# Optimization experiments

Hardware: AMD Instinct MI355X
Metric: run time of the kernel (lower is better)

## Reference

```python
import jax, jax.numpy as jnp
import numpy as np
from math import sqrt

HEADS = 16
DIM_HEAD = 64
BETA = 1.0 / sqrt(DIM_HEAD)


def setup_inputs() -> dict:
    key = jax.random.key(0)
    k1, k2, k3 = jax.random.split(key, 3)
    b, n, dim = 2, 2048, 1024
    inner = HEADS * DIM_HEAD  # 1024
    x = jax.random.normal(k1, (b, n, dim), dtype=jnp.float32)
    W_qk = jax.random.normal(k2, (dim, 2 * inner), dtype=jnp.float32) * 0.02
    W_out = jax.random.normal(k3, (inner, dim), dtype=jnp.float32) * 0.02
    return {"x": x, "W_qk": W_qk, "W_out": W_out}


def reference(x, W_qk, W_out):
    # x: [b, n, dim]; to_qk: Linear(dim, 2*inner, bias=False)
    b, n, _ = x.shape
    qk = x @ W_qk                                   # [b, n, 2*inner]
    q, k = jnp.split(qk, 2, axis=-1)                # each [b, n, inner]
    # b n (h d) -> b h n d
    q = q.reshape(b, n, HEADS, DIM_HEAD).transpose(0, 2, 1, 3)
    k = k.reshape(b, n, HEADS, DIM_HEAD).transpose(0, 2, 1, 3)
    # beta-scaled scores
    scores = jnp.einsum('bhid,bhjd->bhij', q * BETA, k)  # [b, h, n, n]
    mask_value = -jnp.finfo(scores.dtype).max
    causal_mask = jnp.triu(jnp.ones((n, n), dtype=bool), k=1)
    scores = jnp.where(causal_mask, mask_value, scores)
    attn = jax.nn.softmax(scores, axis=-1)
    # K is reused as V
    out = jnp.einsum('bhij,bhjd->bhid', attn, k)    # [b, h, n, d]
    out = out.transpose(0, 2, 1, 3).reshape(b, n, HEADS * DIM_HEAD)
    # to_out Linear (dropout is identity in eval)
    return out @ W_out
```

## Files before the change

### kernel.cpp

```cpp
#include <hip/hip_runtime.h>
#include <hip/hip_bf16.h>
#include <math.h>

typedef short bf16x8 __attribute__((ext_vector_type(8)));
typedef float f32x4 __attribute__((ext_vector_type(4)));

__device__ __forceinline__ float bf2f(unsigned short u) {
    return __uint_as_float(((unsigned int)u) << 16);
}
__device__ __forceinline__ unsigned short f2bf(float f) {
    unsigned int u = __float_as_uint(f);
    u = (u + 0x7FFFu + ((u >> 16) & 1u)) >> 16;
    return (unsigned short)u;
}
__device__ __forceinline__ unsigned int pk2bf(float a, float b) {
    __hip_bfloat162 u = __float22bfloat162_rn(make_float2(a, b));
    return *(unsigned int*)&u;
}

#define ASYNC16(gp, lp)                                                        \
    __builtin_amdgcn_global_load_lds(                                          \
        (const __attribute__((address_space(1))) unsigned int*)(gp),           \
        (__attribute__((address_space(3))) unsigned int*)(lp), 16, 0, 0)

__global__ __launch_bounds__(256) void cast_x_kernel(const float* __restrict__ in,
                                                     unsigned short* __restrict__ out, int n) {
    int i = (blockIdx.x * 256 + threadIdx.x) * 8;
    if (i >= n) return;
    float4 a = *(const float4*)(in + i);
    float4 b = *(const float4*)(in + i + 4);
    bf16x8 v;
    v[0] = (short)f2bf(a.x); v[1] = (short)f2bf(a.y); v[2] = (short)f2bf(a.z); v[3] = (short)f2bf(a.w);
    v[4] = (short)f2bf(b.x); v[5] = (short)f2bf(b.y); v[6] = (short)f2bf(b.z); v[7] = (short)f2bf(b.w);
    *(bf16x8*)(out + i) = v;
}

__global__ __launch_bounds__(256) void transpose_cast_kernel(const float* __restrict__ in,
                                                             unsigned short* __restrict__ out,
                                                             int K, int N) {
    __shared__ float tile[32][33];
    int k0 = blockIdx.x * 32, n0 = blockIdx.y * 32;
    int tx = threadIdx.x & 31, ty = threadIdx.x >> 5;
    #pragma unroll
    for (int i = ty; i < 32; i += 8)
        tile[i][tx] = in[(size_t)(k0 + i) * N + (n0 + tx)];
    __syncthreads();
    #pragma unroll
    for (int i = ty; i < 32; i += 8)
        out[(size_t)(n0 + i) * K + (k0 + tx)] = f2bf(tile[tx][i]);
}

__global__ __launch_bounds__(256) void ktrans_kernel(const unsigned short* __restrict__ qkb,
                                                     unsigned short* __restrict__ kT) {
    __shared__ unsigned short tl[64][68];
    const int b = blockIdx.z;
    const int tok0 = blockIdx.x * 64;
    const int f0 = blockIdx.y * 64;
    const int r = threadIdx.x >> 4;
    const int c = (threadIdx.x & 15) * 4;
    #pragma unroll
    for (int i = 0; i < 4; ++i) {
        const int rr = r + 16 * i;
        ushort4 v = *(const ushort4*)(qkb + ((size_t)(b * 2048 + tok0 + rr)) * 2048 + 1024 + f0 + c);
        *(ushort4*)&tl[rr][c] = v;
    }
    __syncthreads();
    #pragma unroll
    for (int i = 0; i < 4; ++i) {
        const int fr = r + 16 * i;
        ushort4 v;
        v.x = tl[c + 0][fr]; v.y = tl[c + 1][fr]; v.z = tl[c + 2][fr]; v.w = tl[c + 3][fr];
        *(ushort4*)(kT + ((size_t)(b * 1024 + f0 + fr)) * 2048 + tok0 + c) = v;
    }
}

template <bool STORE_BF16>
__global__ __launch_bounds__(256) void gemm128_kernel(const unsigned short* __restrict__ A,
                                                      const unsigned short* __restrict__ Bt,
                                                      void* __restrict__ C,
                                                      int K, int lda, int ldb, int ldc) {
    __shared__ unsigned short As[128 * 32];
    __shared__ unsigned short Bs[128 * 32];
    const int tid = threadIdx.x;
    const int wave = tid >> 6;
    const int lane = tid & 63;
    const int quad = lane >> 4;
    const int col  = lane & 15;
    const int wm = (wave >> 1) * 64;
    const int wn = (wave & 1) * 64;
    const int m0 = blockIdx.x * 128, n0 = blockIdx.y * 128;

    f32x4 acc[4][4];
    #pragma unroll
    for (int i = 0; i < 4; ++i)
        #pragma unroll
        for (int j = 0; j < 4; ++j) { acc[i][j][0] = 0.f; acc[i][j][1] = 0.f; acc[i][j][2] = 0.f; acc[i][j][3] = 0.f; }

    const int srow = tid >> 2;
    const int skc  = (tid & 3) * 8;

    for (int k0 = 0; k0 < K; k0 += 32) {
        __syncthreads();
        const unsigned short* ga = A  + (size_t)(m0 + srow) * lda + k0 + skc;
        const unsigned short* gb = Bt + (size_t)(n0 + srow) * ldb + k0 + skc;
        ASYNC16(ga,            &As[wave * 512]);
        ASYNC16(ga + 64 * lda, &As[2048 + wave * 512]);
        ASYNC16(gb,            &Bs[wave * 512]);
        ASYNC16(gb + 64 * ldb, &Bs[2048 + wave * 512]);
        __syncthreads();

        bf16x8 af[4], bf[4];
        #pragma unroll
        for (int mf = 0; mf < 4; ++mf)
            af[mf] = *(const bf16x8*)&As[(wm + mf * 16 + col) * 32 + quad * 8];
        #pragma unroll
        for (int nf = 0; nf < 4; ++nf)
            bf[nf] = *(const bf16x8*)&Bs[(wn + nf * 16 + col) * 32 + quad * 8];
        #pragma unroll
        for (int mf = 0; mf < 4; ++mf)
            #pragma unroll
            for (int nf = 0; nf < 4; ++nf)
                acc[mf][nf] = __builtin_amdgcn_mfma_f32_16x16x32_bf16(af[mf], bf[nf], acc[mf][nf], 0, 0, 0);
    }

    #pragma unroll
    for (int mf = 0; mf < 4; ++mf) {
        const int row0 = m0 + wm + mf * 16 + quad * 4;
        #pragma unroll
        for (int nf = 0; nf < 4; ++nf) {
            const int cc = n0 + wn + nf * 16 + col;
            #pragma unroll
            for (int r = 0; r < 4; ++r) {
                if (STORE_BF16)
                    ((unsigned short*)C)[(size_t)(row0 + r) * ldc + cc] = f2bf(acc[mf][nf][r]);
                else
                    ((float*)C)[(size_t)(row0 + r) * ldc + cc] = acc[mf][nf][r];
            }
        }
    }
}

#define LDK 72

__global__ __launch_bounds__(256) void attn_v5_kernel(const unsigned short* __restrict__ qkb,
                                                      const unsigned short* __restrict__ kT,
                                                      unsigned short* __restrict__ aout) {
    __shared__ unsigned short Kbuf[2][2][64 * 64];
    __shared__ unsigned short Ps[4][16 * LDK];

    const int bh = blockIdx.x;
    const int b = bh >> 4, h = bh & 15;
    const int qtile = 31 - (int)blockIdx.y;
    const int tid = threadIdx.x;
    const int wave = tid >> 6, lane = tid & 63, quad = lane >> 4, col = lane & 15;

    bf16x8 qa0, qa1;
    {
        const unsigned short* qp =
            qkb + ((size_t)(b * 2048 + qtile * 64 + wave * 16 + col)) * 2048 + h * 64;
        bf16x8 r0 = *(const bf16x8*)(qp + quad * 8);
        bf16x8 r1 = *(const bf16x8*)(qp + 32 + quad * 8);
        const float sc = 0.125f * 1.44269504088896f;
        #pragma unroll
        for (int i = 0; i < 8; ++i) {
            qa0[i] = (short)f2bf(bf2f((unsigned short)r0[i]) * sc);
            qa1[i] = (short)f2bf(bf2f((unsigned short)r1[i]) * sc);
        }
    }

    f32x4 accO[4];
    #pragma unroll
    for (int t = 0; t < 4; ++t) { accO[t][0] = 0.f; accO[t][1] = 0.f; accO[t][2] = 0.f; accO[t][3] = 0.f; }
    float lsum = 0.f;

    const int r8 = lane >> 3;
    const int c8 = (lane & 7) ^ r8;
    const unsigned short* knp =
        qkb + ((size_t)(b * 2048 + wave * 16 + r8)) * 2048 + 1024 + h * 64 + c8 * 8;
    const unsigned short* ktp = kT + ((size_t)(bh * 64 + wave * 16 + r8)) * 2048 + c8 * 8;

    auto issue = [&](int jt, int p) {
        const unsigned short* kn = knp + (size_t)jt * 64 * 2048;
        const unsigned short* kt = ktp + jt * 64;
        unsigned short* knl = &Kbuf[p][0][(wave * 16) * 64];
        unsigned short* ktl = &Kbuf[p][1][(wave * 16) * 64];
        ASYNC16(kn,            knl);
        ASYNC16(kn + 8 * 2048, knl + 8 * 64);
        ASYNC16(kt,            ktl);
        ASYNC16(kt + 8 * 2048, ktl + 8 * 64);
    };

    issue(0, 0);

    for (int jt = 0; jt <= qtile; ++jt) {
        const int cur = jt & 1;
        __builtin_amdgcn_s_barrier();
        if (jt < qtile) issue(jt + 1, cur ^ 1);
        if (jt < qtile) __builtin_amdgcn_s_waitcnt(0xF74);
        else            __builtin_amdgcn_s_waitcnt(0xF70);
        __builtin_amdgcn_s_barrier();
        __asm__ volatile("" ::: "memory");

        const unsigned short* Knc = &Kbuf[cur][0][0];
        const unsigned short* Ktc = &Kbuf[cur][1][0];

        const bool diag = (jt == qtile);
        const int tmax = diag ? wave : 3;

        float ls = 0.f;
        unsigned int pw[4][2];
        #pragma unroll
        for (int t = 0; t < 4; ++t) {
            if (t <= tmax) {
                const int row = (t * 16 + col) * 64;
                const int sw = col & 7;
                bf16x8 ka0 = *(const bf16x8*)&Knc[row + (quad ^ sw) * 8];
                bf16x8 ka1 = *(const bf16x8*)&Knc[row + ((4 + quad) ^ sw) * 8];
                f32x4 c = {-16.f, -16.f, -16.f, -16.f};
                c = __builtin_amdgcn_mfma_f32_16x16x32_bf16(ka0, qa0, c, 0, 0, 0);
                c = __builtin_amdgcn_mfma_f32_16x16x32_bf16(ka1, qa1, c, 0, 0, 0);
                if (diag && t == wave) {
                    #pragma unroll
                    for (int r = 0; r < 4; ++r)
                        if (quad * 4 + r > col) c[r] = -1e30f;
                }
                const float p0 = exp2f(c[0]);
                const float p1 = exp2f(c[1]);
                const float p2 = exp2f(c[2]);
                const float p3 = exp2f(c[3]);
                ls += (p0 + p1) + (p2 + p3);
                pw[t][0] = pk2bf(p0, p1);
                pw[t][1] = pk2bf(p2, p3);
            } else {
                pw[t][0] = 0u; pw[t][1] = 0u;
            }
        }
        lsum += ls;

        unsigned short* psb = &Ps[wave][col * LDK];
        #pragma unroll
        for (int t = 0; t < 4; ++t)
            *(uint2*)(psb + t * 16 + quad * 4) = make_uint2(pw[t][0], pw[t][1]);

        bf16x8 pa0 = *(const bf16x8*)(psb + quad * 8);
        bf16x8 pa1 = *(const bf16x8*)(psb + 32 + quad * 8);
        const bool hi = !(diag && wave < 2);

        #pragma unroll
        for (int t = 0; t < 4; ++t) {
            const int row = (t * 16 + col) * 64;
            const int sw = col & 7;
            bf16x8 vb0 = *(const bf16x8*)&Ktc[row + (quad ^ sw) * 8];
            accO[t] = __builtin_amdgcn_mfma_f32_16x16x32_bf16(pa0, vb0, accO[t], 0, 0, 0);
            if (hi) {
                bf16x8 vb1 = *(const bf16x8*)&Ktc[row + ((4 + quad) ^ sw) * 8];
                accO[t] = __builtin_amdgcn_mfma_f32_16x16x32_bf16(pa1, vb1, accO[t], 0, 0, 0);
            }
        }
    }

    lsum += __shfl_xor(lsum, 16);
    lsum += __shfl_xor(lsum, 32);
    #pragma unroll
    for (int r = 0; r < 4; ++r) {
        const float lr = __shfl(lsum, (lane & 48) | (quad * 4 + r));
        const float inv = 1.f / lr;
        const size_t row = (size_t)b * 2048 + qtile * 64 + wave * 16 + quad * 4 + r;
        unsigned short* op = aout + row * 1024 + h * 64;
        op[col]      = f2bf(accO[0][r] * inv);
        op[16 + col] = f2bf(accO[1][r] * inv);
        op[32 + col] = f2bf(accO[2][r] * inv);
        op[48 + col] = f2bf(accO[3][r] * inv);
    }
}

extern "C" void kernel_launch(void* const* d_in, const int* in_sizes, int n_in,
                              void* d_out, int out_size, void* d_ws, size_t ws_size,
                              hipStream_t stream) {
    (void)in_sizes; (void)n_in; (void)out_size; (void)ws_size;
    const float* x    = (const float*)d_in[0];
    const float* Wqk  = (const float*)d_in[1];
    const float* Wout = (const float*)d_in[2];
    float* out = (float*)d_out;

    unsigned short* xb     = (unsigned short*)d_ws;
    unsigned short* Wqk_t  = xb     + (size_t)4096 * 1024;
    unsigned short* Wout_t = Wqk_t  + (size_t)2048 * 1024;
    unsigned short* qkb    = Wout_t + (size_t)1024 * 1024;
    unsigned short* aoutb  = qkb    + (size_t)4096 * 2048;
    unsigned short* kT     = xb;

    cast_x_kernel<<<dim3(4096 * 1024 / (256 * 8)), dim3(256), 0, stream>>>(x, xb, 4096 * 1024);
    transpose_cast_kernel<<<dim3(32, 64), dim3(256), 0, stream>>>(Wqk, Wqk_t, 1024, 2048);
    transpose_cast_kernel<<<dim3(32, 32), dim3(256), 0, stream>>>(Wout, Wout_t, 1024, 1024);

    gemm128_kernel<true><<<dim3(32, 16), dim3(256), 0, stream>>>(
        xb, Wqk_t, (void*)qkb, 1024, 1024, 1024, 2048);

    ktrans_kernel<<<dim3(32, 16, 2), dim3(256), 0, stream>>>(qkb, kT);

    attn_v5_kernel<<<dim3(32, 32), dim3(256), 0, stream>>>(qkb, kT, aoutb);

    gemm128_kernel<false><<<dim3(32, 8), dim3(256), 0, stream>>>(
        aoutb, Wout_t, (void*)out, 1024, 1024, 1024, 1024);
}
```

Baseline: 196.4 us.

## Process two query tiles per attention block to reuse loaded K tiles

Each attention workgroup now handles 128 query rows: each wave owns two 16-row query sub-tiles, and the grid is halved. Every K/K^T tile staged in LDS is used by both sub-tiles, which halves global-to-LDS K traffic and the barrier count per query row. In exchange, register pressure rises (doubled accumulators and Q fragments) and fewer blocks launch, so occupancy and load balance across CUs may suffer.

```diff
diff --git a/kernel.cpp b/kernel.cpp
--- a/kernel.cpp
+++ b/kernel.cpp
@@ -142,36 +142,39 @@
 
 #define LDK 72
 
-__global__ __launch_bounds__(256) void attn_v5_kernel(const unsigned short* __restrict__ qkb,
+__global__ __launch_bounds__(256) void attn_v6_kernel(const unsigned short* __restrict__ qkb,
                                                       const unsigned short* __restrict__ kT,
                                                       unsigned short* __restrict__ aout) {
     __shared__ unsigned short Kbuf[2][2][64 * 64];
-    __shared__ unsigned short Ps[4][16 * LDK];
+    __shared__ unsigned short Ps[4][32 * LDK];
 
     const int bh = blockIdx.x;
     const int b = bh >> 4, h = bh & 15;
-    const int qtile = 31 - (int)blockIdx.y;
+    const int qtile = 15 - (int)blockIdx.y;
     const int tid = threadIdx.x;
     const int wave = tid >> 6, lane = tid & 63, quad = lane >> 4, col = lane & 15;
 
-    bf16x8 qa0, qa1;
-    {
+    bf16x8 qa[2][2];
+    #pragma unroll
+    for (int s = 0; s < 2; ++s) {
         const unsigned short* qp =
-            qkb + ((size_t)(b * 2048 + qtile * 64 + wave * 16 + col)) * 2048 + h * 64;
+            qkb + ((size_t)(b * 2048 + qtile * 128 + s * 64 + wave * 16 + col)) * 2048 + h * 64;
         bf16x8 r0 = *(const bf16x8*)(qp + quad * 8);
         bf16x8 r1 = *(const bf16x8*)(qp + 32 + quad * 8);
         const float sc = 0.125f * 1.44269504088896f;
         #pragma unroll
         for (int i = 0; i < 8; ++i) {
-            qa0[i] = (short)f2bf(bf2f((unsigned short)r0[i]) * sc);
-            qa1[i] = (short)f2bf(bf2f((unsigned short)r1[i]) * sc);
-        }
-    }
-
-    f32x4 accO[4];
-    #pragma unroll
-    for (int t = 0; t < 4; ++t) { accO[t][0] = 0.f; accO[t][1] = 0.f; accO[t][2] = 0.f; accO[t][3] = 0.f; }
-    float lsum = 0.f;
+            qa[s][0][i] = (short)f2bf(bf2f((unsigned short)r0[i]) * sc);
+            qa[s][1][i] = (short)f2bf(bf2f((unsigned short)r1[i]) * sc);
+        }
+    }
+
+    f32x4 accO[2][4];
+    #pragma unroll
+    for (int s = 0; s < 2; ++s)
+        #pragma unroll
+        for (int t = 0; t < 4; ++t) { accO[s][t][0] = 0.f; accO[s][t][1] = 0.f; accO[s][t][2] = 0.f; accO[s][t][3] = 0.f; }
+    float lsum[2] = {0.f, 0.f};
 
     const int r8 = lane >> 3;
     const int c8 = (lane & 7) ^ r8;
@@ -192,34 +195,45 @@
 
     issue(0, 0);
 
-    for (int jt = 0; jt <= qtile; ++jt) {
+    const int jtmax = 2 * qtile + 1;
+    for (int jt = 0; jt <= jtmax; ++jt) {
         const int cur = jt & 1;
         __builtin_amdgcn_s_barrier();
-        if (jt < qtile) issue(jt + 1, cur ^ 1);
-        if (jt < qtile) __builtin_amdgcn_s_waitcnt(0xF74);
-        else            __builtin_amdgcn_s_waitcnt(0xF70);
+        if (jt < jtmax) {
+            issue(jt + 1, cur ^ 1);
+            __builtin_amdgcn_s_waitcnt(0xF74);
+        } else {
+            __builtin_amdgcn_s_waitcnt(0xF70);
+        }
         __builtin_amdgcn_s_barrier();
         __asm__ volatile("" ::: "memory");
 
         const unsigned short* Knc = &Kbuf[cur][0][0];
         const unsigned short* Ktc = &Kbuf[cur][1][0];
 
-        const bool diag = (jt == qtile);
-        const int tmax = diag ? wave : 3;
-
-        float ls = 0.f;
-        unsigned int pw[4][2];
+        const bool act0 = (jt <= 2 * qtile);
+        const bool dg0  = (jt == 2 * qtile);
+        const bool dg1  = (jt == jtmax);
+        const int tmax0 = dg0 ? wave : 3;
+        const int tmax1 = dg1 ? wave : 3;
+
+        float ls0 = 0.f, ls1 = 0.f;
+        unsigned int pw[2][4][2];
         #pragma unroll
         for (int t = 0; t < 4; ++t) {
-            if (t <= tmax) {
-                const int row = (t * 16 + col) * 64;
-                const int sw = col & 7;
-                bf16x8 ka0 = *(const bf16x8*)&Knc[row + (quad ^ sw) * 8];
-                bf16x8 ka1 = *(const bf16x8*)&Knc[row + ((4 + quad) ^ sw) * 8];
+            const int row = (t * 16 + col) * 64;
+            const int sw = col & 7;
+            const bool need = (!dg1) || (t <= tmax1);
+            bf16x8 ka0 = {}, ka1 = {};
+            if (need) {
+                ka0 = *(const bf16x8*)&Knc[row + (quad ^ sw) * 8];
+                ka1 = *(const bf16x8*)&Knc[row + ((4 + quad) ^ sw) * 8];
+            }
+            if (act0 && t <= tmax0) {
                 f32x4 c = {-16.f, -16.f, -16.f, -16.f};
-                c = __builtin_amdgcn_mfma_f32_16x16x32_bf16(ka0, qa0, c, 0, 0, 0);
-                c = __builtin_amdgcn_mfma_f32_16x16x32_bf16(ka1, qa1, c, 0, 0, 0);
-                if (diag && t == wave) {
+                c = __builtin_amdgcn_mfma_f32_16x16x32_bf16(ka0, qa[0][0], c, 0, 0, 0);
+                c = __builtin_amdgcn_mfma_f32_16x16x32_bf16(ka1, qa[0][1], c, 0, 0, 0);
+                if (dg0 && t == wave) {
                     #pragma unroll
                     for (int r = 0; r < 4; ++r)
                         if (quad * 4 + r > col) c[r] = -1e30f;
@@ -228,49 +242,87 @@
                 const float p1 = exp2f(c[1]);
                 const float p2 = exp2f(c[2]);
                 const float p3 = exp2f(c[3]);
-                ls += (p0 + p1) + (p2 + p3);
-                pw[t][0] = pk2bf(p0, p1);
-                pw[t][1] = pk2bf(p2, p3);
+                ls0 += (p0 + p1) + (p2 + p3);
+                pw[0][t][0] = pk2bf(p0, p1);
+                pw[0][t][1] = pk2bf(p2, p3);
             } else {
-                pw[t][0] = 0u; pw[t][1] = 0u;
-            }
-        }
-        lsum += ls;
-
-        unsigned short* psb = &Ps[wave][col * LDK];
+                pw[0][t][0] = 0u; pw[0][t][1] = 0u;
+            }
+            if (t <= tmax1) {
+                f32x4 c = {-16.f, -16.f, -16.f, -16.f};
+                c = __builtin_amdgcn_mfma_f32_16x16x32_bf16(ka0, qa[1][0], c, 0, 0, 0);
+                c = __builtin_amdgcn_mfma_f32_16x16x32_bf16(ka1, qa[1][1], c, 0, 0, 0);
+                if (dg1 && t == wave) {
+                    #pragma unroll
+                    for (int r = 0; r < 4; ++r)
+                        if (quad * 4 + r > col) c[r] = -1e30f;
+                }
+                const float p0 = exp2f(c[0]);
+                const float p1 = exp2f(c[1]);
+                const float p2 = exp2f(c[2]);
+                const float p3 = exp2f(c[3]);
+                ls1 += (p0 + p1) + (p2 + p3);
+                pw[1][t][0] = pk2bf(p0, p1);
+                pw[1][t][1] = pk2bf(p2, p3);
+            } else {
+                pw[1][t][0] = 0u; pw[1][t][1] = 0u;
+            }
+        }
+        lsum[0] += ls0; lsum[1] += ls1;
+
+        unsigned short* psb0 = &Ps[wave][col * LDK];
+        unsigned short* psb1 = &Ps[wave][(16 + col) * LDK];
+        if (act0) {
+            #pragma unroll
+            for (int t = 0; t < 4; ++t)
+                *(uint2*)(psb0 + t * 16 + quad * 4) = make_uint2(pw[0][t][0], pw[0][t][1]);
+        }
         #pragma unroll
         for (int t = 0; t < 4; ++t)
-            *(uint2*)(psb + t * 16 + quad * 4) = make_uint2(pw[t][0], pw[t][1]);
-
-        bf16x8 pa0 = *(const bf16x8*)(psb + quad * 8);
-        bf16x8 pa1 = *(const bf16x8*)(psb + 32 + quad * 8);
-        const bool hi = !(diag && wave < 2);
+            *(uint2*)(psb1 + t * 16 + quad * 4) = make_uint2(pw[1][t][0], pw[1][t][1]);
+
+        bf16x8 pa00 = {}, pa01 = {};
+        if (act0) {
+            pa00 = *(const bf16x8*)(psb0 + quad * 8);
+            pa01 = *(const bf16x8*)(psb0 + 32 + quad * 8);
+        }
+        bf16x8 pa10 = *(const bf16x8*)(psb1 + quad * 8);
+        bf16x8 pa11 = *(const bf16x8*)(psb1 + 32 + quad * 8);
+        const bool hi0 = act0 && !(dg0 && wave < 2);
+        const bool hi1 = !(dg1 && wave < 2);
 
         #pragma unroll
         for (int t = 0; t < 4; ++t) {
             const int row = (t * 16 + col) * 64;
             const int sw = col & 7;
             bf16x8 vb0 = *(const bf16x8*)&Ktc[row + (quad ^ sw) * 8];
-            accO[t] = __builtin_amdgcn_mfma_f32_16x16x32_bf16(pa0, vb0, accO[t], 0, 0, 0);
-            if (hi) {
+            if (act0) accO[0][t] = __builtin_amdgcn_mfma_f32_16x16x32_bf16(pa00, vb0, accO[0][t], 0, 0, 0);
+            accO[1][t] = __builtin_amdgcn_mfma_f32_16x16x32_bf16(pa10, vb0, accO[1][t], 0, 0, 0);
+            if (hi0 || hi1) {
                 bf16x8 vb1 = *(const bf16x8*)&Ktc[row + ((4 + quad) ^ sw) * 8];
-                accO[t] = __builtin_amdgcn_mfma_f32_16x16x32_bf16(pa1, vb1, accO[t], 0, 0, 0);
-            }
-        }
-    }
-
-    lsum += __shfl_xor(lsum, 16);
-    lsum += __shfl_xor(lsum, 32);
-    #pragma unroll
-    for (int r = 0; r < 4; ++r) {
-        const float lr = __shfl(lsum, (lane & 48) | (quad * 4 + r));
-        const float inv = 1.f / lr;
-        const size_t row = (size_t)b * 2048 + qtile * 64 + wave * 16 + quad * 4 + r;
-        unsigned short* op = aout + row * 1024 + h * 64;
-        op[col]      = f2bf(accO[0][r] * inv);
-        op[16 + col] = f2bf(accO[1][r] * inv);
-        op[32 + col] = f2bf(accO[2][r] * inv);
-        op[48 + col] = f2bf(accO[3][r] * inv);
+                if (hi0) accO[0][t] = __builtin_amdgcn_mfma_f32_16x16x32_bf16(pa01, vb1, accO[0][t], 0, 0, 0);
+                if (hi1) accO[1][t] = __builtin_amdgcn_mfma_f32_16x16x32_bf16(pa11, vb1, accO[1][t], 0, 0, 0);
+            }
+        }
+    }
+
+    #pragma unroll
+    for (int s = 0; s < 2; ++s) {
+        float l = lsum[s];
+        l += __shfl_xor(l, 16);
+        l += __shfl_xor(l, 32);
+        #pragma unroll
+        for (int r = 0; r < 4; ++r) {
+            const float lr = __shfl(l, (lane & 48) | (quad * 4 + r));
+            const float inv = 1.f / lr;
+            const size_t rowg =
+                (size_t)b * 2048 + qtile * 128 + s * 64 + wave * 16 + quad * 4 + r;
+            unsigned short* op = aout + rowg * 1024 + h * 64;
+            op[col]      = f2bf(accO[s][0][r] * inv);
+            op[16 + col] = f2bf(accO[s][1][r] * inv);
+            op[32 + col] = f2bf(accO[s][2][r] * inv);
+            op[48 + col] = f2bf(accO[s][3][r] * inv);
+        }
     }
 }
 
@@ -299,7 +351,7 @@
 
     ktrans_kernel<<<dim3(32, 16, 2), dim3(256), 0, stream>>>(qkb, kT);
 
-    attn_v5_kernel<<<dim3(32, 32), dim3(256), 0, stream>>>(qkb, kT, aoutb);
+    attn_v6_kernel<<<dim3(32, 16), dim3(256), 0, stream>>>(qkb, kT, aoutb);
 
     gemm128_kernel<false><<<dim3(32, 8), dim3(256), 0, stream>>>(
         aoutb, Wout_t, (void*)out, 1024, 1024, 1024, 1024);
```

New measurement: 225.0 us. +14.6%, slower.

## Pair causal query tiles per block to balance attention work

Applied to the files above, without the earlier changes.

Each attention block now processes two query tiles, p and 31-p, one after the other, so every block does the same total number of causal key tiles. The grid shrinks from 32x32 to 32x16 blocks. This removes the load imbalance and tail effect of blocks with very different causal lengths, at the cost of fewer blocks (512 on a 256-CU device) and serial work inside each block. A barrier is added between the two tiles so the shared buffer can be reused.

```diff
diff --git a/kernel.cpp b/kernel.cpp
--- a/kernel.cpp
+++ b/kernel.cpp
@@ -142,7 +142,7 @@
 
 #define LDK 72
 
-__global__ __launch_bounds__(256) void attn_v5_kernel(const unsigned short* __restrict__ qkb,
+__global__ __launch_bounds__(256) void attn_v8_kernel(const unsigned short* __restrict__ qkb,
                                                       const unsigned short* __restrict__ kT,
                                                       unsigned short* __restrict__ aout) {
     __shared__ unsigned short Kbuf[2][2][64 * 64];
@@ -150,28 +150,9 @@
 
     const int bh = blockIdx.x;
     const int b = bh >> 4, h = bh & 15;
-    const int qtile = 31 - (int)blockIdx.y;
+    const int p = (int)blockIdx.y;
     const int tid = threadIdx.x;
     const int wave = tid >> 6, lane = tid & 63, quad = lane >> 4, col = lane & 15;
-
-    bf16x8 qa0, qa1;
-    {
-        const unsigned short* qp =
-            qkb + ((size_t)(b * 2048 + qtile * 64 + wave * 16 + col)) * 2048 + h * 64;
-        bf16x8 r0 = *(const bf16x8*)(qp + quad * 8);
-        bf16x8 r1 = *(const bf16x8*)(qp + 32 + quad * 8);
-        const float sc = 0.125f * 1.44269504088896f;
-        #pragma unroll
-        for (int i = 0; i < 8; ++i) {
-            qa0[i] = (short)f2bf(bf2f((unsigned short)r0[i]) * sc);
-            qa1[i] = (short)f2bf(bf2f((unsigned short)r1[i]) * sc);
-        }
-    }
-
-    f32x4 accO[4];
-    #pragma unroll
-    for (int t = 0; t < 4; ++t) { accO[t][0] = 0.f; accO[t][1] = 0.f; accO[t][2] = 0.f; accO[t][3] = 0.f; }
-    float lsum = 0.f;
 
     const int r8 = lane >> 3;
     const int c8 = (lane & 7) ^ r8;
@@ -179,98 +160,126 @@
         qkb + ((size_t)(b * 2048 + wave * 16 + r8)) * 2048 + 1024 + h * 64 + c8 * 8;
     const unsigned short* ktp = kT + ((size_t)(bh * 64 + wave * 16 + r8)) * 2048 + c8 * 8;
 
-    auto issue = [&](int jt, int p) {
+    auto issue = [&](int jt, int pb) {
         const unsigned short* kn = knp + (size_t)jt * 64 * 2048;
         const unsigned short* kt = ktp + jt * 64;
-        unsigned short* knl = &Kbuf[p][0][(wave * 16) * 64];
-        unsigned short* ktl = &Kbuf[p][1][(wave * 16) * 64];
+        unsigned short* knl = &Kbuf[pb][0][(wave * 16) * 64];
+        unsigned short* ktl = &Kbuf[pb][1][(wave * 16) * 64];
         ASYNC16(kn,            knl);
         ASYNC16(kn + 8 * 2048, knl + 8 * 64);
         ASYNC16(kt,            ktl);
         ASYNC16(kt + 8 * 2048, ktl + 8 * 64);
     };
 
-    issue(0, 0);
-
-    for (int jt = 0; jt <= qtile; ++jt) {
-        const int cur = jt & 1;
-        __builtin_amdgcn_s_barrier();
-        if (jt < qtile) issue(jt + 1, cur ^ 1);
-        if (jt < qtile) __builtin_amdgcn_s_waitcnt(0xF74);
-        else            __builtin_amdgcn_s_waitcnt(0xF70);
-        __builtin_amdgcn_s_barrier();
-        __asm__ volatile("" ::: "memory");
-
-        const unsigned short* Knc = &Kbuf[cur][0][0];
-        const unsigned short* Ktc = &Kbuf[cur][1][0];
-
-        const bool diag = (jt == qtile);
-        const int tmax = diag ? wave : 3;
-
-        float ls = 0.f;
-        unsigned int pw[4][2];
-        #pragma unroll
-        for (int t = 0; t < 4; ++t) {
-            if (t <= tmax) {
+    for (int s = 0; s < 2; ++s) {
+        const int Y = s ? (31 - p) : p;
+
+        if (s) __builtin_amdgcn_s_barrier();
+
+        bf16x8 qa0, qa1;
+        {
+            const unsigned short* qp =
+                qkb + ((size_t)(b * 2048 + Y * 64 + wave * 16 + col)) * 2048 + h * 64;
+            bf16x8 r0 = *(const bf16x8*)(qp + quad * 8);
+            bf16x8 r1 = *(const bf16x8*)(qp + 32 + quad * 8);
+            const float sc = 0.125f * 1.44269504088896f;
+            #pragma unroll
+            for (int i = 0; i < 8; ++i) {
+                qa0[i] = (short)f2bf(bf2f((unsigned short)r0[i]) * sc);
+                qa1[i] = (short)f2bf(bf2f((unsigned short)r1[i]) * sc);
+            }
+        }
+
+        f32x4 accO[4];
+        #pragma unroll
+        for (int t = 0; t < 4; ++t) { accO[t][0] = 0.f; accO[t][1] = 0.f; accO[t][2] = 0.f; accO[t][3] = 0.f; }
+        float lsum = 0.f;
+
+        issue(0, 0);
+
+        for (int jt = 0; jt <= Y; ++jt) {
+            const int cur = jt & 1;
+            __builtin_amdgcn_s_barrier();
+            if (jt < Y) {
+                issue(jt + 1, cur ^ 1);
+                __builtin_amdgcn_s_waitcnt(0xF74);
+            } else {
+                __builtin_amdgcn_s_waitcnt(0xF70);
+            }
+            __builtin_amdgcn_s_barrier();
+            __asm__ volatile("" ::: "memory");
+
+            const unsigned short* Knc = &Kbuf[cur][0][0];
+            const unsigned short* Ktc = &Kbuf[cur][1][0];
+
+            const bool diag = (jt == Y);
+            const int tmax = diag ? wave : 3;
+
+            float ls = 0.f;
+            unsigned int pw[4][2];
+            #pragma unroll
+            for (int t = 0; t < 4; ++t) {
+                if (t <= tmax) {
+                    const int row = (t * 16 + col) * 64;
+                    const int sw = col & 7;
+                    bf16x8 ka0 = *(const bf16x8*)&Knc[row + (quad ^ sw) * 8];
+                    bf16x8 ka1 = *(const bf16x8*)&Knc[row + ((4 + quad) ^ sw) * 8];
+                    f32x4 c = {-16.f, -16.f, -16.f, -16.f};
+                    c = __builtin_amdgcn_mfma_f32_16x16x32_bf16(ka0, qa0, c, 0, 0, 0);
+                    c = __builtin_amdgcn_mfma_f32_16x16x32_bf16(ka1, qa1, c, 0, 0, 0);
+                    if (diag && t == wave) {
+                        #pragma unroll
+                        for (int r = 0; r < 4; ++r)
+                            if (quad * 4 + r > col) c[r] = -1e30f;
+                    }
+                    const float p0 = exp2f(c[0]);
+                    const float p1 = exp2f(c[1]);
+                    const float p2 = exp2f(c[2]);
+                    const float p3 = exp2f(c[3]);
+                    ls += (p0 + p1) + (p2 + p3);
+                    pw[t][0] = pk2bf(p0, p1);
+                    pw[t][1] = pk2bf(p2, p3);
+                } else {
+                    pw[t][0] = 0u; pw[t][1] = 0u;
+                }
+            }
+            lsum += ls;
+
+            unsigned short* psb = &Ps[wave][col * LDK];
+            #pragma unroll
+            for (int t = 0; t < 4; ++t)
+                *(uint2*)(psb + t * 16 + quad * 4) = make_uint2(pw[t][0], pw[t][1]);
+
+            bf16x8 pa0 = *(const bf16x8*)(psb + quad * 8);
+            bf16x8 pa1 = *(const bf16x8*)(psb + 32 + quad * 8);
+            const bool hi = !(diag && wave < 2);
+
+            #pragma unroll
+            for (int t = 0; t < 4; ++t) {
                 const int row = (t * 16 + col) * 64;
                 const int sw = col & 7;
-                bf16x8 ka0 = *(const bf16x8*)&Knc[row + (quad ^ sw) * 8];
-                bf16x8 ka1 = *(const bf16x8*)&Knc[row + ((4 + quad) ^ sw) * 8];
-                f32x4 c = {-16.f, -16.f, -16.f, -16.f};
-                c = __builtin_amdgcn_mfma_f32_16x16x32_bf16(ka0, qa0, c, 0, 0, 0);
-                c = __builtin_amdgcn_mfma_f32_16x16x32_bf16(ka1, qa1, c, 0, 0, 0);
-                if (diag && t == wave) {
-                    #pragma unroll
-                    for (int r = 0; r < 4; ++r)
-                        if (quad * 4 + r > col) c[r] = -1e30f;
+                bf16x8 vb0 = *(const bf16x8*)&Ktc[row + (quad ^ sw) * 8];
+                accO[t] = __builtin_amdgcn_mfma_f32_16x16x32_bf16(pa0, vb0, accO[t], 0, 0, 0);
+                if (hi) {
+                    bf16x8 vb1 = *(const bf16x8*)&Ktc[row + ((4 + quad) ^ sw) * 8];
+                    accO[t] = __builtin_amdgcn_mfma_f32_16x16x32_bf16(pa1, vb1, accO[t], 0, 0, 0);
                 }
-                const float p0 = exp2f(c[0]);
-                const float p1 = exp2f(c[1]);
-                const float p2 = exp2f(c[2]);
-                const float p3 = exp2f(c[3]);
-                ls += (p0 + p1) + (p2 + p3);
-                pw[t][0] = pk2bf(p0, p1);
-                pw[t][1] = pk2bf(p2, p3);
-            } else {
-                pw[t][0] = 0u; pw[t][1] = 0u;
             }
         }
-        lsum += ls;
-
-        unsigned short* psb = &Ps[wave][col * LDK];
-        #pragma unroll
-        for (int t = 0; t < 4; ++t)
-            *(uint2*)(psb + t * 16 + quad * 4) = make_uint2(pw[t][0], pw[t][1]);
-
-        bf16x8 pa0 = *(const bf16x8*)(psb + quad * 8);
-        bf16x8 pa1 = *(const bf16x8*)(psb + 32 + quad * 8);
-        const bool hi = !(diag && wave < 2);
-
-        #pragma unroll
-        for (int t = 0; t < 4; ++t) {
-            const int row = (t * 16 + col) * 64;
-            const int sw = col & 7;
-            bf16x8 vb0 = *(const bf16x8*)&Ktc[row + (quad ^ sw) * 8];
-            accO[t] = __builtin_amdgcn_mfma_f32_16x16x32_bf16(pa0, vb0, accO[t], 0, 0, 0);
-            if (hi) {
-                bf16x8 vb1 = *(const bf16x8*)&Ktc[row + ((4 + quad) ^ sw) * 8];
-                accO[t] = __builtin_amdgcn_mfma_f32_16x16x32_bf16(pa1, vb1, accO[t], 0, 0, 0);
-            }
+
+        lsum += __shfl_xor(lsum, 16);
+        lsum += __shfl_xor(lsum, 32);
+        #pragma unroll
+        for (int r = 0; r < 4; ++r) {
+            const float lr = __shfl(lsum, (lane & 48) | (quad * 4 + r));
+            const float inv = 1.f / lr;
+            const size_t row = (size_t)b * 2048 + Y * 64 + wave * 16 + quad * 4 + r;
+            unsigned short* op = aout + row * 1024 + h * 64;
+            op[col]      = f2bf(accO[0][r] * inv);
+            op[16 + col] = f2bf(accO[1][r] * inv);
+            op[32 + col] = f2bf(accO[2][r] * inv);
+            op[48 + col] = f2bf(accO[3][r] * inv);
         }
-    }
-
-    lsum += __shfl_xor(lsum, 16);
-    lsum += __shfl_xor(lsum, 32);
-    #pragma unroll
-    for (int r = 0; r < 4; ++r) {
-        const float lr = __shfl(lsum, (lane & 48) | (quad * 4 + r));
-        const float inv = 1.f / lr;
-        const size_t row = (size_t)b * 2048 + qtile * 64 + wave * 16 + quad * 4 + r;
-        unsigned short* op = aout + row * 1024 + h * 64;
-        op[col]      = f2bf(accO[0][r] * inv);
-        op[16 + col] = f2bf(accO[1][r] * inv);
-        op[32 + col] = f2bf(accO[2][r] * inv);
-        op[48 + col] = f2bf(accO[3][r] * inv);
     }
 }
 
@@ -299,7 +308,7 @@
 
     ktrans_kernel<<<dim3(32, 16, 2), dim3(256), 0, stream>>>(qkb, kT);
 
-    attn_v5_kernel<<<dim3(32, 32), dim3(256), 0, stream>>>(qkb, kT, aoutb);
+    attn_v8_kernel<<<dim3(32, 16), dim3(256), 0, stream>>>(qkb, kT, aoutb);
 
     gemm128_kernel<false><<<dim3(32, 8), dim3(256), 0, stream>>>(
         aoutb, Wout_t, (void*)out, 1024, 1024, 1024, 1024);
```

Measured after the change: 201.2 us. +2.5%, slower.
